# Kernel optimization log

Measured on AMD Instinct MI355X. Metric: run time of the kernel, lower is better.

Reference implementation:

```python
import jax, jax.numpy as jnp
import numpy as np

N = 65536      # active voxels
K = 27         # 3x3x3 SubM kernel taps
CIN = 4        # input voxel features (x,y,z,intensity)
C = 32         # stage-1 channels
NW = 2048      # number of attention windows
CAP = 32       # padded voxels per window (NW*CAP == N)
H = 2          # attention heads
HD = C // H    # head dim
R = 144        # quantized relative-position bins


def _subm_conv(feats, pairs, w):
    # spconv SubMConv3d as gather-scatter: pairs[k, i] = input voxel feeding
    # kernel tap k of output voxel i, or -1 if that neighbor is empty.
    valid = pairs >= 0                      # [K, N]
    idx = jnp.where(valid, pairs, 0)
    g = feats[idx] * valid[:, :, None].astype(feats.dtype)   # [K, N, Cin]
    return jnp.einsum('knc,kcd->nd', g, w)                    # [N, Cout]


def _bn_relu(x, g, b):
    # BatchNorm1d (eval, running stats folded) + ReLU
    return jax.nn.relu(x * g + b)


def _res_block(x, pairs, g1, b1, w1, g2, b2, w2):
    h = _bn_relu(x, g1, b1)
    h = _subm_conv(h, pairs, w1)
    h = _bn_relu(h, g2, b2)
    h = _subm_conv(h, pairs, w2)
    return x + h  # identity branch (in_ch == out_ch)


def _sphere_attention(x, win_idx, rel_idx, w_qkv, b_qkv, w_proj, b_proj, tq, tk, tv):
    xw = x[win_idx]                                           # [NW, CAP, C]
    qkv = (xw @ w_qkv + b_qkv).reshape(NW, CAP, 3, H, HD)
    q = qkv[:, :, 0] * (HD ** -0.5)
    k = qkv[:, :, 1]
    v = qkv[:, :, 2]
    scores = jnp.einsum('wihd,wjhd->whij', q, k)              # [NW, H, CAP, CAP]
    # quantized relative-position contributions (rel_query / rel_key)
    rq = tq[rel_idx]                                          # [NW, CAP, CAP, H, HD]
    rk = tk[rel_idx]
    scores = scores + jnp.einsum('wihd,wijhd->whij', q, rq)
    scores = scores + jnp.einsum('wjhd,wijhd->whij', k, rk)
    attn = jax.nn.softmax(scores, axis=-1)
    out = jnp.einsum('whij,wjhd->wihd', attn, v)
    out = out + jnp.einsum('whij,wijhd->wihd', attn, tv[rel_idx])  # rel_value
    out = out.reshape(NW, CAP, C) @ w_proj + b_proj
    # scatter windows back to the flat voxel list (win_idx is a permutation)
    y = jnp.zeros_like(x).at[win_idx.reshape(-1)].set(out.reshape(-1, C))
    return x + y  # residual (drop_path=0 in stage 1)


def setup_inputs() -> dict:
    key = jax.random.key(0)
    ks = jax.random.split(key, 16)
    feats = jax.random.normal(ks[0], (N, CIN), dtype=jnp.float32)
    pairs = jax.random.randint(ks[1], (K, N), 0, N, dtype=jnp.int32)
    drop = jax.random.uniform(ks[2], (K, N)) < 0.3
    pairs = jnp.where(drop, -1, pairs)
    pairs = pairs.at[K // 2].set(jnp.arange(N, dtype=jnp.int32))  # center tap = self
    win_idx = jax.random.permutation(ks[3], N).reshape(NW, CAP).astype(jnp.int32)
    rel_idx = jax.random.randint(ks[4], (NW, CAP, CAP), 0, R, dtype=jnp.int32)

    def w(k, shape, s=0.05):
        return jax.random.normal(k, shape, dtype=jnp.float32) * s

    wk = jax.random.split(ks[5], 12)
    inp = dict(feats=feats, pairs=pairs, win_idx=win_idx, rel_idx=rel_idx,
               w_in=w(wk[0], (K, CIN, C)),
               rb1_g1=jnp.ones((C,)), rb1_b1=jnp.zeros((C,)), rb1_w1=w(wk[1], (K, C, C)),
               rb1_g2=jnp.ones((C,)), rb1_b2=jnp.zeros((C,)), rb1_w2=w(wk[2], (K, C, C)),
               rb2_g1=jnp.ones((C,)), rb2_b1=jnp.zeros((C,)), rb2_w1=w(wk[3], (K, C, C)),
               rb2_g2=jnp.ones((C,)), rb2_b2=jnp.zeros((C,)), rb2_w2=w(wk[4], (K, C, C)),
               w_qkv=w(wk[5], (C, 3 * C), 0.1), b_qkv=jnp.zeros((3 * C,)),
               w_proj=w(wk[6], (C, C), 0.1), b_proj=jnp.zeros((C,)),
               tq=w(wk[7], (R, H, HD)), tk=w(wk[8], (R, H, HD)), tv=w(wk[9], (R, H, HD)))
    return inp


def reference(feats, pairs, win_idx, rel_idx, w_in,
              rb1_g1, rb1_b1, rb1_w1, rb1_g2, rb1_b2, rb1_w2,
              rb2_g1, rb2_b1, rb2_w1, rb2_g2, rb2_b2, rb2_w2,
              w_qkv, b_qkv, w_proj, b_proj, tq, tk, tv):
    x = _subm_conv(feats, pairs, w_in)                       # input_conv
    x = _res_block(x, pairs, rb1_g1, rb1_b1, rb1_w1, rb1_g2, rb1_b2, rb1_w2)
    x = _res_block(x, pairs, rb2_g1, rb2_b1, rb2_w1, rb2_g2, rb2_b2, rb2_w2)
    x = _sphere_attention(x, win_idx, rel_idx, w_qkv, b_qkv, w_proj, b_proj, tq, tk, tv)
    return x
```

## Files before the change

kernel.cpp:

```cpp
#include <hip/hip_runtime.h>

typedef unsigned short u16;
typedef unsigned int u32;

#define N_PTS 65536
#define KK 27
#define CIN 4
#define CC 32
#define NWIN 2048
#define CAP 32
#define NH 2
#define HD 16

typedef short s16x8 __attribute__((ext_vector_type(8)));
typedef float f32x4 __attribute__((ext_vector_type(4)));

__device__ __forceinline__ float bf2f(u16 h) { return __uint_as_float(((u32)h) << 16); }
__device__ __forceinline__ u16 f2bf(float f) {
    u32 u = __float_as_uint(f);
    u32 r = (u + 0x7FFFu + ((u >> 16) & 1u)) >> 16;
    return (u16)r;
}
__device__ __forceinline__ float ldany(const void* src, int i, bool isbf) {
    return isbf ? bf2f(((const u16*)src)[i]) : ((const float*)src)[i];
}
__device__ __forceinline__ u16 ldbf(const void* src, int i, bool isbf) {
    return isbf ? ((const u16*)src)[i] : f2bf(((const float*)src)[i]);
}

__global__ void detect_kernel(const u32* __restrict__ w, int* flag) {
    int t = threadIdx.x;
    int cnt = 0;
    for (int i = t; i < 4096; i += 256) {
        u32 e = (w[i] >> 7) & 0xFFu;
        cnt += (e >= 100 && e <= 140) ? 1 : 0;
    }
    __shared__ int red[256];
    red[t] = cnt;
    __syncthreads();
    for (int s = 128; s > 0; s >>= 1) {
        if (t < s) red[t] += red[t + s];
        __syncthreads();
    }
    if (t == 0) flag[0] = (red[0] > 2048) ? 1 : 0;
}

struct Ptrs { const void* p[24]; };

__global__ __launch_bounds__(256) void prep_all(
    Ptrs in, const int* __restrict__ flag,
    u16* __restrict__ fbf,
    u16* __restrict__ WpA1, u16* __restrict__ WpA2,
    u16* __restrict__ WpB1, u16* __restrict__ WpB2, u16* __restrict__ WpIN,
    u16* __restrict__ wqkvB, u16* __restrict__ wprojB,
    u16* __restrict__ tqB, u16* __restrict__ tkB, u16* __restrict__ tvb,
    float* __restrict__ Pf)
{
    bool isbf = flag[0] != 0;
    int seg = blockIdx.y;
    int i = blockIdx.x * 256 + threadIdx.x;
    if (seg == 0) {
        if (i < N_PTS * CIN) fbf[i] = ldbf(in.p[0], i, isbf);
        return;
    }
    if (seg <= 4) {
        if (i < 27648) {
            int e = i & 7, l = (i >> 3) & 63, dt = (i >> 9) & 1, k = i >> 10;
            const void* src = in.p[seg == 1 ? 7 : seg == 2 ? 10 : seg == 3 ? 13 : 16];
            u16* dst = seg == 1 ? WpA1 : seg == 2 ? WpA2 : seg == 3 ? WpB1 : WpB2;
            dst[i] = ldbf(src, k * 1024 + ((l >> 4) * 8 + e) * 32 + dt * 16 + (l & 15), isbf);
        }
        return;
    }
    if (seg == 5) {
        if (i < 4096) {
            int e = i & 7, l = (i >> 3) & 63, dt = (i >> 9) & 1, kk = i >> 10;
            int g = kk * 32 + (l >> 4) * 8 + e;
            int tp = g >> 2, c = g & 3;
            WpIN[i] = (tp < KK) ? ldbf(in.p[4], tp * 128 + c * 32 + dt * 16 + (l & 15), isbf) : (u16)0;
        }
        return;
    }
    if (seg == 6) {
        if (i < 3072) {
            int e = i & 7, l = (i >> 3) & 63, n = i >> 9;
            wqkvB[i] = ldbf(in.p[17], ((l >> 4) * 8 + e) * 96 + n * 16 + (l & 15), isbf);
        } else if (i < 4096) {
            int o2 = i - 3072;
            int e = o2 & 7, l = (o2 >> 3) & 63, n = o2 >> 9;
            wprojB[o2] = ldbf(in.p[19], ((l >> 4) * 8 + e) * 32 + n * 16 + (l & 15), isbf);
        }
        return;
    }
    if (seg == 7) {
        if (i < 9216) {
            int e = i & 7, l = (i >> 3) & 63, nn = i >> 9;
            int n = nn % 9, h = nn / 9, lr = l & 15, lg = l >> 4;
            int k = lg * 8 + e;
            tqB[i] = (k < HD) ? ldbf(in.p[21], (n * 16 + lr) * 32 + h * 16 + k, isbf) : (u16)0;
        } else if (i < 18432) {
            int o2 = i - 9216;
            int e = o2 & 7, l = (o2 >> 3) & 63, nn = o2 >> 9;
            int n = nn % 9, h = nn / 9, lr = l & 15, lg = l >> 4;
            int k = lg * 8 + e;
            tkB[o2] = (k < HD) ? ldbf(in.p[22], (n * 16 + lr) * 32 + h * 16 + k, isbf) : (u16)0;
        } else if (i < 23040) {
            int o2 = i - 18432;
            tvb[o2] = ldbf(in.p[23], o2, isbf);
        }
        return;
    }
    if (i < 256) {
        const int srcs[8] = {5, 6, 8, 9, 11, 12, 14, 15};
        Pf[i] = ldany(in.p[srcs[i >> 5]], i & 31, isbf);
    } else if (i < 352) {
        Pf[i] = ldany(in.p[18], i - 256, isbf);
    } else if (i < 384) {
        Pf[i] = ldany(in.p[20], i - 352, isbf);
    }
}

__global__ __launch_bounds__(256) void convin_mfma(
    const u16* __restrict__ fb, const int* __restrict__ pairs,
    const u16* __restrict__ Wp, const float* __restrict__ gb,
    float* __restrict__ xbuf, u16* __restrict__ act_out)
{
    int t = threadIdx.x;
    int wv = t >> 6, l = t & 63;
    int lr = l & 15, lg = l >> 4;
    int p0 = (blockIdx.x * 4 + wv) * 16;
    int rowaddr = p0 + lr;

    int ia[4], ib[4];
    u32 ma[4], mb[4];
#pragma unroll
    for (int kk = 0; kk < 4; kk++) {
        int t0 = kk * 8 + lg * 2;
        int ta = t0 < 26 ? t0 : 26;
        int tb = (t0 + 1) < 26 ? (t0 + 1) : 26;
        ia[kk] = pairs[ta * N_PTS + rowaddr];
        ib[kk] = pairs[tb * N_PTS + rowaddr];
        ma[kk] = (t0 < KK && ia[kk] >= 0) ? 0xFFFFFFFFu : 0u;
        mb[kk] = (t0 + 1 < KK && ib[kk] >= 0) ? 0xFFFFFFFFu : 0u;
    }
    uint2 qa[4], qb[4];
    s16x8 b0[4], b1[4];
#pragma unroll
    for (int kk = 0; kk < 4; kk++) {
        qa[kk] = *(const uint2*)(fb + (long)(ia[kk] < 0 ? 0 : ia[kk]) * CIN);
        qb[kk] = *(const uint2*)(fb + (long)(ib[kk] < 0 ? 0 : ib[kk]) * CIN);
        const s16x8* wb = (const s16x8*)Wp + kk * 128 + l;
        b0[kk] = wb[0];
        b1[kk] = wb[64];
    }

    f32x4 acc0 = {0.f, 0.f, 0.f, 0.f}, acc1 = {0.f, 0.f, 0.f, 0.f};
#pragma unroll
    for (int kk = 0; kk < 4; kk++) {
        union { uint4 q; s16x8 v; } a;
        a.q = make_uint4(qa[kk].x & ma[kk], qa[kk].y & ma[kk],
                         qb[kk].x & mb[kk], qb[kk].y & mb[kk]);
        acc0 = __builtin_amdgcn_mfma_f32_16x16x32_bf16(a.v, b0[kk], acc0, 0, 0, 0);
        acc1 = __builtin_amdgcn_mfma_f32_16x16x32_bf16(a.v, b1[kk], acc1, 0, 0, 0);
    }
    float g0 = gb[lr], b0v = gb[32 + lr], g1 = gb[16 + lr], b1v = gb[48 + lr];
#pragma unroll
    for (int r = 0; r < 4; r++) {
        int row = p0 + lg * 4 + r;
        long o0 = (long)row * 32 + lr, o1 = o0 + 16;
        float v0 = acc0[r], v1 = acc1[r];
        xbuf[o0] = v0; xbuf[o1] = v1;
        act_out[o0] = f2bf(fmaxf(fmaf(v0, g0, b0v), 0.f));
        act_out[o1] = f2bf(fmaxf(fmaf(v1, g1, b1v), 0.f));
    }
}

template <int M>
__global__ __launch_bounds__(512, 4) void conv32_lds(
    const u16* __restrict__ act_in, const int* __restrict__ pairs,
    const u16* __restrict__ Wp, const float* __restrict__ gb,
    float* __restrict__ xbuf, u16* __restrict__ act_out)
{
    __shared__ u16 wlds[KK * 1024];
    int t = threadIdx.x;
    int wv = t >> 6, l = t & 63;
    int lr = l & 15, lg = l >> 4;

    {
        const uint4* src = (const uint4*)Wp;
        uint4* dst = (uint4*)wlds;
#pragma unroll
        for (int q = 0; q < 7; q++) {
            int e = q * 512 + t;
            if (e < 3456) dst[e] = src[e];
        }
    }
    __syncthreads();

    float g0 = 0.f, b0v = 0.f, g1 = 0.f, b1v = 0.f;
    if (M & 4) { g0 = gb[lr]; b0v = gb[32 + lr]; g1 = gb[16 + lr]; b1v = gb[48 + lr]; }

#pragma unroll
    for (int tile = 0; tile < 2; tile++) {
        int p0 = ((blockIdx.x * 8 + wv) * 2 + tile) * 16;
        int rowaddr = p0 + lr;

        int idx[KK];
#pragma unroll
        for (int k = 0; k < KK; k++) idx[k] = pairs[k * N_PTS + rowaddr];

        uint4 qr[8];
#pragma unroll
        for (int k = 0; k < 8; k++) {
            int ic = idx[k] < 0 ? 0 : idx[k];
            qr[k] = *(const uint4*)(act_in + (long)ic * CC + lg * 8);
        }

        f32x4 acc0 = {0.f, 0.f, 0.f, 0.f}, acc1 = {0.f, 0.f, 0.f, 0.f};
#pragma unroll
        for (int k = 0; k < KK; k++) {
            int s = k & 7;
            uint4 q = qr[s];
            if (k + 8 < KK) {
                int kn = k + 8;
                int ic = idx[kn] < 0 ? 0 : idx[kn];
                qr[s] = *(const uint4*)(act_in + (long)ic * CC + lg * 8);
            }
            u32 msk = idx[k] >= 0 ? 0xFFFFFFFFu : 0u;
            q.x &= msk; q.y &= msk; q.z &= msk; q.w &= msk;
            union { uint4 q; s16x8 v; } a;
            a.q = q;
            const s16x8* wb = (const s16x8*)wlds + k * 128 + l;
            s16x8 w0 = wb[0];
            s16x8 w1 = wb[64];
            acc0 = __builtin_amdgcn_mfma_f32_16x16x32_bf16(a.v, w0, acc0, 0, 0, 0);
            acc1 = __builtin_amdgcn_mfma_f32_16x16x32_bf16(a.v, w1, acc1, 0, 0, 0);
        }
#pragma unroll
        for (int r = 0; r < 4; r++) {
            int row = p0 + lg * 4 + r;
            long o0 = (long)row * 32 + lr, o1 = o0 + 16;
            float v0 = acc0[r], v1 = acc1[r];
            if (M & 1) { v0 += xbuf[o0]; v1 += xbuf[o1]; }
            if (M & 2) { xbuf[o0] = v0; xbuf[o1] = v1; }
            if (M & 4) {
                act_out[o0] = f2bf(fmaxf(fmaf(v0, g0, b0v), 0.f));
                act_out[o1] = f2bf(fmaxf(fmaf(v1, g1, b1v), 0.f));
            }
        }
    }
}

#define A5_RIDX 0
#define A5_QSB  4096
#define A5_KSB  6656
#define A5_VST  9216
#define A5_SC   11776
#define A5_BQ   20992
#define A5_BK   30208
#define A5_SIZE 39424

__global__ __launch_bounds__(512) void attn6_kernel(
    const float* __restrict__ x, const int* __restrict__ win_idx,
    const int* __restrict__ rel_idx,
    const u16* __restrict__ wqkvB, const u16* __restrict__ wprojB,
    const float* __restrict__ Pf,
    const u16* __restrict__ tqB, const u16* __restrict__ tkB, const u16* __restrict__ tvb,
    float* __restrict__ out)
{
    __shared__ __align__(16) char arena2[2][A5_SIZE];
    int t = threadIdx.x;
    int wl = t >> 8;
    int tl = t & 255;
    int w = blockIdx.x * 2 + wl;
    char* arena = arena2[wl];

    int*   ridx = (int*)(arena + A5_RIDX);
    u16*   qsb  = (u16*)(arena + A5_QSB);
    u16*   ksb  = (u16*)(arena + A5_KSB);
    u16*   vsT  = (u16*)(arena + A5_VST);
    float* sc   = (float*)(arena + A5_SC);
    u16*   psb  = (u16*)(arena + A5_SC);
    u16*   Bq   = (u16*)(arena + A5_BQ);
    u16*   Bk   = (u16*)(arena + A5_BK);
    float* ot   = (float*)(arena + A5_BQ);

    int wv = tl >> 6, l = tl & 63, lr = l & 15, lg = l >> 4;

    {
        int4 r4 = *(const int4*)(rel_idx + (long)w * 1024 + tl * 4);
        *(int4*)(ridx + tl * 4) = r4;
    }
    {
        const float* bqkv = Pf + 256;
        for (int pi = wv; pi < 12; pi += 4) {
            int n = pi >> 1, m = pi & 1;
            int gi = win_idx[w * 32 + m * 16 + lr];
            const float* xr = x + (long)gi * 32 + lg * 8;
            float4 x0 = *(const float4*)(xr);
            float4 x1 = *(const float4*)(xr + 4);
            union { s16x8 v; u16 h[8]; } a;
            a.h[0] = f2bf(x0.x); a.h[1] = f2bf(x0.y); a.h[2] = f2bf(x0.z); a.h[3] = f2bf(x0.w);
            a.h[4] = f2bf(x1.x); a.h[5] = f2bf(x1.y); a.h[6] = f2bf(x1.z); a.h[7] = f2bf(x1.w);
            s16x8 b = *(const s16x8*)(wqkvB + ((n * 64 + l) << 3));
            f32x4 acc = {0.f, 0.f, 0.f, 0.f};
            acc = __builtin_amdgcn_mfma_f32_16x16x32_bf16(a.v, b, acc, 0, 0, 0);
            int tt = n * 16 + lr;
            float bias = bqkv[tt];
#pragma unroll
            for (int r = 0; r < 4; r++) {
                int tok = m * 16 + lg * 4 + r;
                float v = acc[r] + bias;
                if (tt < 32)      qsb[tok * 40 + tt] = f2bf(v * 0.25f);
                else if (tt < 64) ksb[tok * 40 + (tt - 32)] = f2bf(v);
                else              vsT[(tt - 64) * 40 + tok] = f2bf(v);
            }
        }
    }
    __syncthreads();

    for (int h = 0; h < NH; h++) {
        {
            int tb = wv >> 1, m = wv & 1;
            const u16* src = tb ? ksb : qsb;
            const u16* tab = tb ? tkB : tqB;
            u16* dst = tb ? Bk : Bq;
            s16x8 a = {0, 0, 0, 0, 0, 0, 0, 0};
            if (lg < 2) a = *(const s16x8*)(src + (m * 16 + lr) * 40 + h * 16 + lg * 8);
#pragma unroll
            for (int n = 0; n < 9; n++) {
                s16x8 b = *(const s16x8*)(tab + (((h * 9 + n) * 64 + l) << 3));
                f32x4 acc = {0.f, 0.f, 0.f, 0.f};
                acc = __builtin_amdgcn_mfma_f32_16x16x32_bf16(a, b, acc, 0, 0, 0);
#pragma unroll
                for (int r = 0; r < 4; r++)
                    dst[(m * 16 + lg * 4 + r) * 144 + n * 16 + lr] = f2bf(acc[r]);
            }
        }
        __syncthreads();
        for (int e = tl; e < 1024; e += 256) {
            int i = e >> 5, j = e & 31, r = ridx[e];
            sc[h * 1152 + i * 36 + j] = bf2f(Bq[i * 144 + r]) + bf2f(Bk[j * 144 + r]);
        }
        __syncthreads();
    }

    for (int pi = wv; pi < 8; pi += 4) {
        int h = pi >> 2, m = (pi >> 1) & 1, n = pi & 1;
        s16x8 a = {0, 0, 0, 0, 0, 0, 0, 0}, b = {0, 0, 0, 0, 0, 0, 0, 0};
        if (lg < 2) {
            a = *(const s16x8*)(qsb + (m * 16 + lr) * 40 + h * 16 + lg * 8);
            b = *(const s16x8*)(ksb + (n * 16 + lr) * 40 + h * 16 + lg * 8);
        }
        f32x4 acc = {0.f, 0.f, 0.f, 0.f};
        acc = __builtin_amdgcn_mfma_f32_16x16x32_bf16(a, b, acc, 0, 0, 0);
#pragma unroll
        for (int r = 0; r < 4; r++)
            sc[h * 1152 + (m * 16 + lg * 4 + r) * 36 + n * 16 + lr] += acc[r];
    }
    __syncthreads();

    {
        int rr = tl >> 2, sub = tl & 3;
        int h = rr >> 5, i = rr & 31, j0 = sub * 8;
        const float* srow = sc + h * 1152 + i * 36 + j0;
        float pv[8];
        float m_ = -1e30f;
#pragma unroll
        for (int jj = 0; jj < 8; jj++) { pv[jj] = srow[jj]; m_ = fmaxf(m_, pv[jj]); }
        m_ = fmaxf(m_, __shfl_xor(m_, 1));
        m_ = fmaxf(m_, __shfl_xor(m_, 2));
        float sum = 0.f;
#pragma unroll
        for (int jj = 0; jj < 8; jj++) { pv[jj] = __expf(pv[jj] - m_); sum += pv[jj]; }
        sum += __shfl_xor(sum, 1);
        sum += __shfl_xor(sum, 2);
        float inv = 1.f / sum;
        __syncthreads();
        u16* prow = psb + h * 1280 + i * 40 + j0;
#pragma unroll
        for (int jj = 0; jj < 8; jj++) prow[jj] = f2bf(pv[jj] * inv);
    }
    __syncthreads();

    for (int o = tl; o < CAP * 16; o += 256) {
        int i = o >> 4, hp = o & 15, h = hp >> 3;
        const u16* prow = psb + h * 1280 + i * 40;
        const int* rrow = ridx + i * 32;
        float a0 = 0.f, a1 = 0.f;
#pragma unroll 8
        for (int j = 0; j < CAP; j++) {
            int r = rrow[j];
            float p = bf2f(prow[j]);
            u32 tv2 = *(const u32*)(tvb + r * 32 + hp * 2);
            a0 = fmaf(p, __uint_as_float(tv2 << 16), a0);
            a1 = fmaf(p, __uint_as_float(tv2 & 0xffff0000u), a1);
        }
        ot[i * 36 + hp * 2] = a0;
        ot[i * 36 + hp * 2 + 1] = a1;
    }
    __syncthreads();

    {
        int h = wv >> 1, m = wv & 1;
        s16x8 a = *(const s16x8*)(psb + h * 1280 + (m * 16 + lr) * 40 + lg * 8);
        s16x8 b = *(const s16x8*)(vsT + (h * 16 + lr) * 40 + lg * 8);
        f32x4 acc = {0.f, 0.f, 0.f, 0.f};
        acc = __builtin_amdgcn_mfma_f32_16x16x32_bf16(a, b, acc, 0, 0, 0);
#pragma unroll
        for (int r = 0; r < 4; r++)
            ot[(m * 16 + lg * 4 + r) * 36 + h * 16 + lr] += acc[r];
    }
    __syncthreads();

    {
        int m = wv >> 1, n = wv & 1;
        union { s16x8 v; u16 h[8]; } a;
        const float* orow = ot + (m * 16 + lr) * 36 + lg * 8;
#pragma unroll
        for (int e = 0; e < 8; e++) a.h[e] = f2bf(orow[e]);
        s16x8 b = *(const s16x8*)(wprojB + ((n * 64 + l) << 3));
        f32x4 acc = {0.f, 0.f, 0.f, 0.f};
        acc = __builtin_amdgcn_mfma_f32_16x16x32_bf16(a.v, b, acc, 0, 0, 0);
        int c = n * 16 + lr;
        float bb = Pf[352 + c];
#pragma unroll
        for (int r = 0; r < 4; r++) {
            int tok = m * 16 + lg * 4 + r;
            int gi = win_idx[w * 32 + tok];
            out[(long)gi * 32 + c] = x[(long)gi * 32 + c] + bb + acc[r];
        }
    }
}

#define B_PF     0
#define B_FLAG   1536
#define B_ACTA   2048
#define B_ACTB   4196352
#define B_FEATS  8390656
#define B_WA1    8914944
#define B_WA2    8970240
#define B_WB1    9025536
#define B_WB2    9080832
#define B_WIN    9136128
#define B_WQKVB  9144320
#define B_WPROJB 9150464
#define B_TQBF   9152512
#define B_TKBF   9170944
#define B_TVBF   9189376

extern "C" void kernel_launch(void* const* d_in, const int* in_sizes, int n_in,
                              void* d_out, int out_size, void* d_ws, size_t ws_size,
                              hipStream_t stream) {
    const void* feats  = d_in[0];
    const int* pairs   = (const int*)d_in[1];
    const int* win_idx = (const int*)d_in[2];
    const int* rel_idx = (const int*)d_in[3];

    char* wsb = (char*)d_ws;
    float* Pf = (float*)(wsb + B_PF);
    int* flag = (int*)(wsb + B_FLAG);
    u16* actA = (u16*)(wsb + B_ACTA);
    u16* actB = (u16*)(wsb + B_ACTB);
    u16* fbf  = (u16*)(wsb + B_FEATS);
    u16* WpA1 = (u16*)(wsb + B_WA1);
    u16* WpA2 = (u16*)(wsb + B_WA2);
    u16* WpB1 = (u16*)(wsb + B_WB1);
    u16* WpB2 = (u16*)(wsb + B_WB2);
    u16* WpIN = (u16*)(wsb + B_WIN);
    u16* wqkvB  = (u16*)(wsb + B_WQKVB);
    u16* wprojB = (u16*)(wsb + B_WPROJB);
    u16* tqB = (u16*)(wsb + B_TQBF);
    u16* tkB = (u16*)(wsb + B_TKBF);
    u16* tvb = (u16*)(wsb + B_TVBF);
    float* X  = (float*)d_out;

    detect_kernel<<<1, 256, 0, stream>>>((const u32*)feats, flag);

    Ptrs pp;
    for (int i = 0; i < 24; i++) pp.p[i] = d_in[i];
    prep_all<<<dim3(1024, 9), 256, 0, stream>>>(pp, flag, fbf,
                                                WpA1, WpA2, WpB1, WpB2, WpIN,
                                                wqkvB, wprojB, tqB, tkB, tvb, Pf);

    convin_mfma<<<1024, 256, 0, stream>>>(fbf, pairs, WpIN, Pf + 0, X, actA);
    conv32_lds<4><<<256, 512, 0, stream>>>(actA, pairs, WpA1, Pf + 64,  X, actB);
    conv32_lds<7><<<256, 512, 0, stream>>>(actB, pairs, WpA2, Pf + 128, X, actA);
    conv32_lds<4><<<256, 512, 0, stream>>>(actA, pairs, WpB1, Pf + 192, X, actB);
    conv32_lds<3><<<256, 512, 0, stream>>>(actB, pairs, WpB2, Pf, X, actA);

    attn6_kernel<<<NWIN / 2, 512, 0, stream>>>(X, win_idx, rel_idx,
                                               wqkvB, wprojB, Pf,
                                               tqB, tkB, tvb, X);
}
```

Measured before the change: 113.4 us.

## Fold dtype detection into prep, raise conv occupancy, one window per attention block

Removes the separate dtype-detection launch and recomputes the flag per block inside prep_all from a smaller sample of the input. The conv kernels drop the 27-entry index register array for a validity bitmask and reload pair indices, trim the LDS weight buffer to 26 taps (the last tap is read from global memory), and raise the occupancy hint from 4 to 6. The attention kernel now processes one window per 512-thread block instead of two per block, spreading each stage's work over eight waves. The aim is less launch overhead and fewer registers for more resident waves, at the cost of extra global reloads and per-block detection work.

```diff
diff --git a/kernel.cpp b/kernel.cpp
--- a/kernel.cpp
+++ b/kernel.cpp
@@ -28,27 +28,10 @@
     return isbf ? ((const u16*)src)[i] : f2bf(((const float*)src)[i]);
 }
 
-__global__ void detect_kernel(const u32* __restrict__ w, int* flag) {
-    int t = threadIdx.x;
-    int cnt = 0;
-    for (int i = t; i < 4096; i += 256) {
-        u32 e = (w[i] >> 7) & 0xFFu;
-        cnt += (e >= 100 && e <= 140) ? 1 : 0;
-    }
-    __shared__ int red[256];
-    red[t] = cnt;
-    __syncthreads();
-    for (int s = 128; s > 0; s >>= 1) {
-        if (t < s) red[t] += red[t + s];
-        __syncthreads();
-    }
-    if (t == 0) flag[0] = (red[0] > 2048) ? 1 : 0;
-}
-
 struct Ptrs { const void* p[24]; };
 
 __global__ __launch_bounds__(256) void prep_all(
-    Ptrs in, const int* __restrict__ flag,
+    Ptrs in,
     u16* __restrict__ fbf,
     u16* __restrict__ WpA1, u16* __restrict__ WpA2,
     u16* __restrict__ WpB1, u16* __restrict__ WpB2, u16* __restrict__ WpIN,
@@ -56,9 +39,22 @@
     u16* __restrict__ tqB, u16* __restrict__ tkB, u16* __restrict__ tvb,
     float* __restrict__ Pf)
 {
-    bool isbf = flag[0] != 0;
+    __shared__ int red[256];
+    int t = threadIdx.x;
+    {
+        u32 wd = ((const u32*)in.p[0])[t];
+        u32 e = (wd >> 7) & 0xFFu;
+        red[t] = (e >= 100 && e <= 140) ? 1 : 0;
+    }
+    __syncthreads();
+    for (int s = 128; s > 0; s >>= 1) {
+        if (t < s) red[t] += red[t + s];
+        __syncthreads();
+    }
+    bool isbf = red[0] > 128;
+
     int seg = blockIdx.y;
-    int i = blockIdx.x * 256 + threadIdx.x;
+    int i = blockIdx.x * 256 + t;
     if (seg == 0) {
         if (i < N_PTS * CIN) fbf[i] = ldbf(in.p[0], i, isbf);
         return;
@@ -176,12 +172,12 @@
 }
 
 template <int M>
-__global__ __launch_bounds__(512, 4) void conv32_lds(
+__global__ __launch_bounds__(512, 6) void conv32_lds(
     const u16* __restrict__ act_in, const int* __restrict__ pairs,
     const u16* __restrict__ Wp, const float* __restrict__ gb,
     float* __restrict__ xbuf, u16* __restrict__ act_out)
 {
-    __shared__ u16 wlds[KK * 1024];
+    __shared__ u16 wlds[26 * 1024];
     int t = threadIdx.x;
     int wv = t >> 6, l = t & 63;
     int lr = l & 15, lg = l >> 4;
@@ -192,7 +188,7 @@
 #pragma unroll
         for (int q = 0; q < 7; q++) {
             int e = q * 512 + t;
-            if (e < 3456) dst[e] = src[e];
+            if (e < 3328) dst[e] = src[e];
         }
     }
     __syncthreads();
@@ -205,15 +201,13 @@
         int p0 = ((blockIdx.x * 8 + wv) * 2 + tile) * 16;
         int rowaddr = p0 + lr;
 
-        int idx[KK];
-#pragma unroll
-        for (int k = 0; k < KK; k++) idx[k] = pairs[k * N_PTS + rowaddr];
-
+        u32 mbits = 0;
         uint4 qr[8];
 #pragma unroll
-        for (int k = 0; k < 8; k++) {
-            int ic = idx[k] < 0 ? 0 : idx[k];
-            qr[k] = *(const uint4*)(act_in + (long)ic * CC + lg * 8);
+        for (int k = 0; k < KK; k++) {
+            int id = pairs[k * N_PTS + rowaddr];
+            mbits |= (id >= 0 ? 1u : 0u) << k;
+            if (k < 8) qr[k] = *(const uint4*)(act_in + (long)(id < 0 ? 0 : id) * CC + lg * 8);
         }
 
         f32x4 acc0 = {0.f, 0.f, 0.f, 0.f}, acc1 = {0.f, 0.f, 0.f, 0.f};
@@ -223,14 +217,15 @@
             uint4 q = qr[s];
             if (k + 8 < KK) {
                 int kn = k + 8;
-                int ic = idx[kn] < 0 ? 0 : idx[kn];
-                qr[s] = *(const uint4*)(act_in + (long)ic * CC + lg * 8);
+                int id = pairs[kn * N_PTS + rowaddr];
+                qr[s] = *(const uint4*)(act_in + (long)(id < 0 ? 0 : id) * CC + lg * 8);
             }
-            u32 msk = idx[k] >= 0 ? 0xFFFFFFFFu : 0u;
+            u32 msk = (mbits >> k) & 1u ? 0xFFFFFFFFu : 0u;
             q.x &= msk; q.y &= msk; q.z &= msk; q.w &= msk;
             union { uint4 q; s16x8 v; } a;
             a.q = q;
-            const s16x8* wb = (const s16x8*)wlds + k * 128 + l;
+            const s16x8* wb = (k < 26) ? ((const s16x8*)wlds + k * 128 + l)
+                                       : ((const s16x8*)Wp + 26 * 128 + l);
             s16x8 w0 = wb[0];
             s16x8 w1 = wb[64];
             acc0 = __builtin_amdgcn_mfma_f32_16x16x32_bf16(a.v, w0, acc0, 0, 0, 0);
@@ -260,7 +255,7 @@
 #define A5_BK   30208
 #define A5_SIZE 39424
 
-__global__ __launch_bounds__(512) void attn6_kernel(
+__global__ __launch_bounds__(512, 8) void attn7_kernel(
     const float* __restrict__ x, const int* __restrict__ win_idx,
     const int* __restrict__ rel_idx,
     const u16* __restrict__ wqkvB, const u16* __restrict__ wprojB,
@@ -268,13 +263,7 @@
     const u16* __restrict__ tqB, const u16* __restrict__ tkB, const u16* __restrict__ tvb,
     float* __restrict__ out)
 {
-    __shared__ __align__(16) char arena2[2][A5_SIZE];
-    int t = threadIdx.x;
-    int wl = t >> 8;
-    int tl = t & 255;
-    int w = blockIdx.x * 2 + wl;
-    char* arena = arena2[wl];
-
+    __shared__ __align__(16) char arena[A5_SIZE];
     int*   ridx = (int*)(arena + A5_RIDX);
     u16*   qsb  = (u16*)(arena + A5_QSB);
     u16*   ksb  = (u16*)(arena + A5_KSB);
@@ -285,15 +274,16 @@
     u16*   Bk   = (u16*)(arena + A5_BK);
     float* ot   = (float*)(arena + A5_BQ);
 
-    int wv = tl >> 6, l = tl & 63, lr = l & 15, lg = l >> 4;
-
-    {
-        int4 r4 = *(const int4*)(rel_idx + (long)w * 1024 + tl * 4);
-        *(int4*)(ridx + tl * 4) = r4;
+    int w = blockIdx.x, t = threadIdx.x;
+    int wv = t >> 6, l = t & 63, lr = l & 15, lg = l >> 4;
+
+    if (t < 256) {
+        int4 r4 = *(const int4*)(rel_idx + (long)w * 1024 + t * 4);
+        *(int4*)(ridx + t * 4) = r4;
     }
     {
         const float* bqkv = Pf + 256;
-        for (int pi = wv; pi < 12; pi += 4) {
+        for (int pi = wv; pi < 12; pi += 8) {
             int n = pi >> 1, m = pi & 1;
             int gi = win_idx[w * 32 + m * 16 + lr];
             const float* xr = x + (long)gi * 32 + lg * 8;
@@ -321,14 +311,14 @@
 
     for (int h = 0; h < NH; h++) {
         {
-            int tb = wv >> 1, m = wv & 1;
+            int tb = (wv >> 2) & 1, m = (wv >> 1) & 1, nh = wv & 1;
             const u16* src = tb ? ksb : qsb;
             const u16* tab = tb ? tkB : tqB;
             u16* dst = tb ? Bk : Bq;
             s16x8 a = {0, 0, 0, 0, 0, 0, 0, 0};
             if (lg < 2) a = *(const s16x8*)(src + (m * 16 + lr) * 40 + h * 16 + lg * 8);
-#pragma unroll
-            for (int n = 0; n < 9; n++) {
+            int n0 = nh * 5, n1 = nh ? 9 : 5;
+            for (int n = n0; n < n1; n++) {
                 s16x8 b = *(const s16x8*)(tab + (((h * 9 + n) * 64 + l) << 3));
                 f32x4 acc = {0.f, 0.f, 0.f, 0.f};
                 acc = __builtin_amdgcn_mfma_f32_16x16x32_bf16(a, b, acc, 0, 0, 0);
@@ -338,15 +328,15 @@
             }
         }
         __syncthreads();
-        for (int e = tl; e < 1024; e += 256) {
+        for (int e = t; e < 1024; e += 512) {
             int i = e >> 5, j = e & 31, r = ridx[e];
             sc[h * 1152 + i * 36 + j] = bf2f(Bq[i * 144 + r]) + bf2f(Bk[j * 144 + r]);
         }
         __syncthreads();
     }
 
-    for (int pi = wv; pi < 8; pi += 4) {
-        int h = pi >> 2, m = (pi >> 1) & 1, n = pi & 1;
+    {
+        int h = wv >> 2, m = (wv >> 1) & 1, n = wv & 1;
         s16x8 a = {0, 0, 0, 0, 0, 0, 0, 0}, b = {0, 0, 0, 0, 0, 0, 0, 0};
         if (lg < 2) {
             a = *(const s16x8*)(qsb + (m * 16 + lr) * 40 + h * 16 + lg * 8);
@@ -361,30 +351,32 @@
     __syncthreads();
 
     {
-        int rr = tl >> 2, sub = tl & 3;
-        int h = rr >> 5, i = rr & 31, j0 = sub * 8;
+        int rr = t >> 3, sub = t & 7;
+        int h = rr >> 5, i = rr & 31, j0 = sub * 4;
         const float* srow = sc + h * 1152 + i * 36 + j0;
-        float pv[8];
+        float pv[4];
         float m_ = -1e30f;
 #pragma unroll
-        for (int jj = 0; jj < 8; jj++) { pv[jj] = srow[jj]; m_ = fmaxf(m_, pv[jj]); }
+        for (int jj = 0; jj < 4; jj++) { pv[jj] = srow[jj]; m_ = fmaxf(m_, pv[jj]); }
         m_ = fmaxf(m_, __shfl_xor(m_, 1));
         m_ = fmaxf(m_, __shfl_xor(m_, 2));
+        m_ = fmaxf(m_, __shfl_xor(m_, 4));
         float sum = 0.f;
 #pragma unroll
-        for (int jj = 0; jj < 8; jj++) { pv[jj] = __expf(pv[jj] - m_); sum += pv[jj]; }
+        for (int jj = 0; jj < 4; jj++) { pv[jj] = __expf(pv[jj] - m_); sum += pv[jj]; }
         sum += __shfl_xor(sum, 1);
         sum += __shfl_xor(sum, 2);
+        sum += __shfl_xor(sum, 4);
         float inv = 1.f / sum;
         __syncthreads();
         u16* prow = psb + h * 1280 + i * 40 + j0;
 #pragma unroll
-        for (int jj = 0; jj < 8; jj++) prow[jj] = f2bf(pv[jj] * inv);
-    }
-    __syncthreads();
-
-    for (int o = tl; o < CAP * 16; o += 256) {
-        int i = o >> 4, hp = o & 15, h = hp >> 3;
+        for (int jj = 0; jj < 4; jj++) prow[jj] = f2bf(pv[jj] * inv);
+    }
+    __syncthreads();
+
+    {
+        int i = t >> 4, hp = t & 15, h = hp >> 3;
         const u16* prow = psb + h * 1280 + i * 40;
         const int* rrow = ridx + i * 32;
         float a0 = 0.f, a1 = 0.f;
@@ -401,7 +393,7 @@
     }
     __syncthreads();
 
-    {
+    if (wv < 4) {
         int h = wv >> 1, m = wv & 1;
         s16x8 a = *(const s16x8*)(psb + h * 1280 + (m * 16 + lr) * 40 + lg * 8);
         s16x8 b = *(const s16x8*)(vsT + (h * 16 + lr) * 40 + lg * 8);
@@ -413,8 +405,8 @@
     }
     __syncthreads();
 
-    {
-        int m = wv >> 1, n = wv & 1;
+    if (wv >= 4) {
+        int m = (wv >> 1) & 1, n = wv & 1;
         union { s16x8 v; u16 h[8]; } a;
         const float* orow = ot + (m * 16 + lr) * 36 + lg * 8;
 #pragma unroll
@@ -434,7 +426,6 @@
 }
 
 #define B_PF     0
-#define B_FLAG   1536
 #define B_ACTA   2048
 #define B_ACTB   4196352
 #define B_FEATS  8390656
@@ -456,10 +447,10 @@
     const int* pairs   = (const int*)d_in[1];
     const int* win_idx = (const int*)d_in[2];
     const int* rel_idx = (const int*)d_in[3];
+    (void)feats;
 
     char* wsb = (char*)d_ws;
     float* Pf = (float*)(wsb + B_PF);
-    int* flag = (int*)(wsb + B_FLAG);
     u16* actA = (u16*)(wsb + B_ACTA);
     u16* actB = (u16*)(wsb + B_ACTB);
     u16* fbf  = (u16*)(wsb + B_FEATS);
@@ -475,11 +466,9 @@
     u16* tvb = (u16*)(wsb + B_TVBF);
     float* X  = (float*)d_out;
 
-    detect_kernel<<<1, 256, 0, stream>>>((const u32*)feats, flag);
-
     Ptrs pp;
     for (int i = 0; i < 24; i++) pp.p[i] = d_in[i];
-    prep_all<<<dim3(1024, 9), 256, 0, stream>>>(pp, flag, fbf,
+    prep_all<<<dim3(1024, 9), 256, 0, stream>>>(pp, fbf,
                                                 WpA1, WpA2, WpB1, WpB2, WpIN,
                                                 wqkvB, wprojB, tqB, tkB, tvb, Pf);
 
@@ -489,7 +478,7 @@
     conv32_lds<4><<<256, 512, 0, stream>>>(actA, pairs, WpB1, Pf + 192, X, actB);
     conv32_lds<3><<<256, 512, 0, stream>>>(actB, pairs, WpB2, Pf, X, actA);
 
-    attn6_kernel<<<NWIN / 2, 512, 0, stream>>>(X, win_idx, rel_idx,
-                                               wqkvB, wprojB, Pf,
-                                               tqB, tkB, tvb, X);
-}
+    attn7_kernel<<<NWIN, 512, 0, stream>>>(X, win_idx, rel_idx,
+                                           wqkvB, wprojB, Pf,
+                                           tqB, tkB, tvb, X);
+}
```

Result: slower. 149.1 us (+31.5%).
